# Performance work log

Hardware: AMD Instinct MI355X
Metric: run time of the kernel (lower is better)

## Reference

```python
import jax, jax.numpy as jnp
import numpy as np

B, N, C, H = 8, 1024, 768, 12
HD = C // H
SCALE = HD ** -0.5


def setup_inputs() -> dict:
    key = jax.random.key(0)
    k1, k2, k3 = jax.random.split(key, 3)
    x = jax.random.normal(k1, (B, N, C), dtype=jnp.float32)
    # parameter init roughly matching nn.Linear default scale
    w_qkv = jax.random.normal(k2, (C, 3 * C), dtype=jnp.float32) * (C ** -0.5)
    w_out = jax.random.normal(k3, (C, C), dtype=jnp.float32) * (C ** -0.5)
    b_out = jnp.zeros((C,), dtype=jnp.float32)
    return {"x": x, "w_qkv": w_qkv, "w_out": w_out, "b_out": b_out}


def reference(x, w_qkv, w_out, b_out):
    b, n, c = x.shape
    qkv = x @ w_qkv                                   # [b, n, 3c]
    q, k, v = jnp.split(qkv, 3, axis=-1)
    # [b, n, c] -> [b, heads, n, head_dim]
    def to_heads(t):
        return t.reshape(b, n, H, HD).transpose(0, 2, 1, 3)
    q, k, v = to_heads(q), to_heads(k), to_heads(v)
    dots = jnp.einsum('bhqd,bhkd->bhqk', q, k) * SCALE  # [b, h, n, n]
    attn = jax.nn.softmax(dots, axis=-1)
    # dropout is identity in eval mode
    out = jnp.einsum('bhqk,bhkd->bhqd', attn, v)        # [b, h, n, hd]
    out = out.transpose(0, 2, 1, 3).reshape(b, n, c)
    return out @ w_out + b_out
```

## Files before the change

### kernel.cpp

```cpp
#include <hip/hip_runtime.h>
#include <stdint.h>


typedef __attribute__((ext_vector_type(8))) __bf16 bf16x8;
typedef __attribute__((ext_vector_type(4))) float f32x4;

__device__ __forceinline__ uint16_t f2bf(float f) {
    union { float f; unsigned u; } c; c.f = f;
    unsigned x = c.u;
    unsigned r = (x + 0x7FFFu + ((x >> 16) & 1u)) >> 16;
    return (uint16_t)r;
}

__device__ __forceinline__ void gload_lds16(const uint16_t* g, uint16_t* l) {
    __builtin_amdgcn_global_load_lds(
        (const __attribute__((address_space(1))) unsigned int*)g,
        (__attribute__((address_space(3))) unsigned int*)l, 16, 0, 0);
}

__global__ __launch_bounds__(256) void cvt_f32_bf16(
    const float* __restrict__ src, uint16_t* __restrict__ dst, int n) {
    int i = (blockIdx.x * 256 + threadIdx.x) * 8;
    if (i + 8 > n) return;
    float4 a = *(const float4*)(src + i);
    float4 b = *(const float4*)(src + i + 4);
    union { uint16_t u[8]; uint4 v; } o;
    o.u[0] = f2bf(a.x); o.u[1] = f2bf(a.y); o.u[2] = f2bf(a.z); o.u[3] = f2bf(a.w);
    o.u[4] = f2bf(b.x); o.u[5] = f2bf(b.y); o.u[6] = f2bf(b.z); o.u[7] = f2bf(b.w);
    *(uint4*)(dst + i) = o.v;
}

__global__ void transpose_f32_bf16(const float* __restrict__ src,
                                   uint16_t* __restrict__ dst, int R, int Cc) {
    __shared__ uint16_t tile[32][33];
    int tx = threadIdx.x, ty = threadIdx.y;
    int c0 = blockIdx.x * 32, r0 = blockIdx.y * 32;
#pragma unroll
    for (int i = 0; i < 4; i++) {
        int r = ty + i * 8;
        tile[r][tx] = f2bf(src[(size_t)(r0 + r) * Cc + c0 + tx]);
    }
    __syncthreads();
#pragma unroll
    for (int i = 0; i < 4; i++) {
        int r = ty + i * 8;
        dst[(size_t)(c0 + r) * R + r0 + tx] = tile[tx][r];
    }
}

template <int MODE>
__global__ __launch_bounds__(256) void gemm128(
    const uint16_t* __restrict__ A, const uint16_t* __restrict__ Bt,
    int Kdim, int Ncols,
    uint16_t* __restrict__ qws, uint16_t* __restrict__ kws,
    uint16_t* __restrict__ vtws,
    const float* __restrict__ bias, float* __restrict__ outp) {
    __shared__ uint16_t lA[2][2][2048];
    __shared__ uint16_t lB[2][2][4096];

    int tid = threadIdx.x;
    int w = tid >> 6, lane = tid & 63, quad = lane >> 4, lo = lane & 15;
    int mw = w >> 1, nw = w & 1;
    int m0 = blockIdx.y * 64;
    int n0 = blockIdx.x * 128;

    int srow = tid >> 2;
    int skc = ((tid & 3) ^ ((tid >> 3) & 3)) * 8;
    const uint16_t* gA0 = A + (size_t)(m0 + srow) * Kdim + skc;
    const uint16_t* gB0 = Bt + (size_t)(n0 + srow) * Kdim + skc;
    const uint16_t* gB1 = gB0 + (size_t)64 * Kdim;

    f32x4 acc[2][4];
#pragma unroll
    for (int i = 0; i < 2; i++)
#pragma unroll
        for (int j = 0; j < 4; j++) acc[i][j] = (f32x4){0.f, 0.f, 0.f, 0.f};

    int swz = (quad ^ ((lo >> 1) & 3)) * 8;
    int aoff = (mw * 32 + lo) * 32 + swz;
    int boff = (nw * 64 + lo) * 32 + swz;

    const int nIter = Kdim >> 6;

#pragma unroll
    for (int s = 0; s < 2; s++) {
        gload_lds16(gA0 + s * 32, &lA[0][s][tid * 8]);
        gload_lds16(gB0 + s * 32, &lB[0][s][tid * 8]);
        gload_lds16(gB1 + s * 32, &lB[0][s][2048 + tid * 8]);
    }
    __syncthreads();

    for (int it = 0; it < nIter; it++) {
        const int cur = it & 1, nxt = cur ^ 1;
        const int kn = (it + 1 < nIter) ? (it + 1) * 64 : 0;

#pragma unroll
        for (int s = 0; s < 2; s++) {
            gload_lds16(gA0 + kn + s * 32, &lA[nxt][s][tid * 8]);
            gload_lds16(gB0 + kn + s * 32, &lB[nxt][s][tid * 8]);
            gload_lds16(gB1 + kn + s * 32, &lB[nxt][s][2048 + tid * 8]);
        }

#pragma unroll
        for (int s = 0; s < 2; s++) {
            bf16x8 af[2], bfr[4];
#pragma unroll
            for (int i = 0; i < 2; i++) af[i] = *(const bf16x8*)(&lA[cur][s][aoff + i * 512]);
#pragma unroll
            for (int j = 0; j < 4; j++) bfr[j] = *(const bf16x8*)(&lB[cur][s][boff + j * 512]);
#pragma unroll
            for (int i = 0; i < 2; i++)
#pragma unroll
                for (int j = 0; j < 4; j++)
                    acc[i][j] = __builtin_amdgcn_mfma_f32_16x16x32_bf16(
                        af[i], bfr[j], acc[i][j], 0, 0, 0);
        }
        __syncthreads();
    }

    if (MODE == 0) {
        int part = n0 / 768;
        int ccb = n0 % 768 + nw * 64;
        float qsc = (part == 0) ? 0.18033688011112042f : 1.0f;
#pragma unroll
        for (int i = 0; i < 2; i++)
#pragma unroll
            for (int j = 0; j < 4; j++)
#pragma unroll
                for (int r = 0; r < 4; r++) {
                    int m = m0 + mw * 32 + i * 16 + quad * 4 + r;
                    int bidx = m >> 10, nidx = m & 1023;
                    int cc = ccb + j * 16 + lo;
                    int h = cc >> 6, d = cc & 63;
                    int bh = bidx * 12 + h;
                    uint16_t v = f2bf(acc[i][j][r] * qsc);
                    int kt = nidx >> 5, keyin = nidx & 31;
                    if (part == 0) {
                        qws[((size_t)bh * 1024 + nidx) * 64 + d] = v;
                    } else if (part == 1) {
                        int fs = ((d >> 5) << 1) | (keyin & 1);
                        int idx = ((bh << 5) + kt) * 2048 + fs * 512 +
                                  ((((d & 31) >> 3) << 4) + (keyin >> 1)) * 8 + (d & 7);
                        kws[idx] = v;
                    } else {
                        int idx = ((bh << 5) + kt) * 2048 + (d >> 4) * 512 +
                                  (((keyin >> 3) << 4) + (d & 15)) * 8 + (keyin & 7);
                        vtws[idx] = v;
                    }
                }
    } else {
#pragma unroll
        for (int i = 0; i < 2; i++)
#pragma unroll
            for (int j = 0; j < 4; j++)
#pragma unroll
                for (int r = 0; r < 4; r++) {
                    int m = m0 + mw * 32 + i * 16 + quad * 4 + r;
                    int c = n0 + nw * 64 + j * 16 + lo;
                    outp[(size_t)m * Ncols + c] = acc[i][j][r] + bias[c];
                }
    }
}

__global__ __launch_bounds__(256) void attn_kernel(
    const uint16_t* __restrict__ qws, const uint16_t* __restrict__ kws,
    const uint16_t* __restrict__ vtws, uint16_t* __restrict__ attnout) {
    int bh = blockIdx.x;
    int qt = blockIdx.y;
    int tid = threadIdx.x;
    int w = tid >> 6, lane = tid & 63, quad = lane >> 4, lo = lane & 15;
    int q0 = qt * 128 + w * 32;

    const uint16_t* Qb = qws + (size_t)bh * 65536;
    const uint16_t* Kt = kws + (size_t)bh * 65536;
    const uint16_t* Vt = vtws + (size_t)bh * 65536;

    bf16x8 aq[2][2];
#pragma unroll
    for (int rg = 0; rg < 2; rg++)
#pragma unroll
        for (int h = 0; h < 2; h++)
            aq[rg][h] = *(const bf16x8*)(Qb + (size_t)(q0 + rg * 16 + lo) * 64 + h * 32 + quad * 8);

    f32x4 oacc[2][4], ol[2];
#pragma unroll
    for (int rg = 0; rg < 2; rg++) {
        ol[rg] = (f32x4){0.f, 0.f, 0.f, 0.f};
#pragma unroll
        for (int nd = 0; nd < 4; nd++) oacc[rg][nd] = (f32x4){0.f, 0.f, 0.f, 0.f};
    }

    bf16x8 ones;
#pragma unroll
    for (int i = 0; i < 8; i++) ones[i] = (__bf16)1.0f;

    __shared__ uint16_t P[4][2][16][40];

    const f32x4 zero4 = (f32x4){0.f, 0.f, 0.f, 0.f};

#pragma unroll 2
    for (int kt = 0; kt < 32; kt++) {
        const uint16_t* Kb = Kt + kt * 2048;
        const uint16_t* Vb = Vt + kt * 2048;

        bf16x8 bk[2][2], vv[4];
#pragma unroll
        for (int t = 0; t < 2; t++)
#pragma unroll
            for (int h = 0; h < 2; h++)
                bk[t][h] = *(const bf16x8*)(Kb + (h * 2 + t) * 512 + lane * 8);
#pragma unroll
        for (int nd = 0; nd < 4; nd++)
            vv[nd] = *(const bf16x8*)(Vb + nd * 512 + lane * 8);

#pragma unroll
        for (int rg = 0; rg < 2; rg++) {
            f32x4 s0 = __builtin_amdgcn_mfma_f32_16x16x32_bf16(aq[rg][0], bk[0][0], zero4, 0, 0, 0);
            s0 = __builtin_amdgcn_mfma_f32_16x16x32_bf16(aq[rg][1], bk[0][1], s0, 0, 0, 0);
            f32x4 s1 = __builtin_amdgcn_mfma_f32_16x16x32_bf16(aq[rg][0], bk[1][0], zero4, 0, 0, 0);
            s1 = __builtin_amdgcn_mfma_f32_16x16x32_bf16(aq[rg][1], bk[1][1], s1, 0, 0, 0);
#pragma unroll
            for (int r = 0; r < 4; r++) {
                union { float f; unsigned u; } u0, u1;
                u0.f = __builtin_exp2f(s0[r]);
                u1.f = __builtin_exp2f(s1[r]);
                unsigned pk = __builtin_amdgcn_perm(u1.u, u0.u, 0x07060302u);
                *(unsigned*)&P[w][rg][quad * 4 + r][2 * lo] = pk;
            }
        }

#pragma unroll
        for (int rg = 0; rg < 2; rg++) {
            bf16x8 ap = *(const bf16x8*)(&P[w][rg][lo][quad * 8]);
            ol[rg] = __builtin_amdgcn_mfma_f32_16x16x32_bf16(ap, ones, ol[rg], 0, 0, 0);
#pragma unroll
            for (int nd = 0; nd < 4; nd++)
                oacc[rg][nd] = __builtin_amdgcn_mfma_f32_16x16x32_bf16(ap, vv[nd], oacc[rg][nd], 0, 0, 0);
        }
    }

    int b = bh / 12, hh = bh % 12;
#pragma unroll
    for (int rg = 0; rg < 2; rg++)
#pragma unroll
        for (int r = 0; r < 4; r++) {
            float inv = 1.0f / ol[rg][r];
            int n = q0 + rg * 16 + quad * 4 + r;
            size_t base = ((size_t)(b * 1024 + n)) * 768 + hh * 64;
#pragma unroll
            for (int nd = 0; nd < 4; nd++)
                attnout[base + nd * 16 + lo] = f2bf(oacc[rg][nd][r] * inv);
        }
}

extern "C" void kernel_launch(void* const* d_in, const int* in_sizes, int n_in,
                              void* d_out, int out_size, void* d_ws, size_t ws_size,
                              hipStream_t stream) {
    const float* x     = (const float*)d_in[0];
    const float* w_qkv = (const float*)d_in[1];
    const float* w_out = (const float*)d_in[2];
    const float* b_out = (const float*)d_in[3];
    float* out = (float*)d_out;

    char* ws = (char*)d_ws;
    uint16_t* xbf   = (uint16_t*)(ws);
    uint16_t* qws   = (uint16_t*)(ws + 12582912);
    uint16_t* kws   = (uint16_t*)(ws + 25165824);
    uint16_t* vtws  = (uint16_t*)(ws + 37748736);
    uint16_t* attn  = (uint16_t*)(ws + 50331648);
    uint16_t* wtqkv = (uint16_t*)(ws + 62914560);
    uint16_t* wtout = (uint16_t*)(ws + 66453504);

    cvt_f32_bf16<<<6291456 / 2048, 256, 0, stream>>>(x, xbf, 6291456);

    transpose_f32_bf16<<<dim3(2304 / 32, 768 / 32), dim3(32, 8), 0, stream>>>(w_qkv, wtqkv, 768, 2304);
    transpose_f32_bf16<<<dim3(768 / 32, 768 / 32), dim3(32, 8), 0, stream>>>(w_out, wtout, 768, 768);

    gemm128<0><<<dim3(18, 128), 256, 0, stream>>>(
        xbf, wtqkv, 768, 2304, qws, kws, vtws, nullptr, nullptr);

    attn_kernel<<<dim3(96, 8), 256, 0, stream>>>(qws, kws, vtws, attn);

    gemm128<1><<<dim3(6, 128), 256, 0, stream>>>(
        attn, wtout, 768, 768, nullptr, nullptr, nullptr, b_out, out);
}
```

Measured before the change: 209.7 us.

## Merge prep kernels into one launch and swizzle GEMM workgroup order

Three preprocessing kernels (x conversion and two weight transposes) are folded into a single prep launch that dispatches by block index, removing two kernel launches and their gaps. The GEMM kernels also remap the linear workgroup id into an XCD-style interleaved order, so that blocks placed on the same chiplet work on neighbouring tiles and share L2. The remap assumes the grid size is divisible by 8, which holds for both GEMM launches.

New measurement: 198.8 us. 1.05x faster.

```diff
diff --git a/kernel.cpp b/kernel.cpp
--- a/kernel.cpp
+++ b/kernel.cpp
@@ -18,23 +18,38 @@
         (__attribute__((address_space(3))) unsigned int*)l, 16, 0, 0);
 }
 
-__global__ __launch_bounds__(256) void cvt_f32_bf16(
-    const float* __restrict__ src, uint16_t* __restrict__ dst, int n) {
-    int i = (blockIdx.x * 256 + threadIdx.x) * 8;
-    if (i + 8 > n) return;
-    float4 a = *(const float4*)(src + i);
-    float4 b = *(const float4*)(src + i + 4);
-    union { uint16_t u[8]; uint4 v; } o;
-    o.u[0] = f2bf(a.x); o.u[1] = f2bf(a.y); o.u[2] = f2bf(a.z); o.u[3] = f2bf(a.w);
-    o.u[4] = f2bf(b.x); o.u[5] = f2bf(b.y); o.u[6] = f2bf(b.z); o.u[7] = f2bf(b.w);
-    *(uint4*)(dst + i) = o.v;
-}
-
-__global__ void transpose_f32_bf16(const float* __restrict__ src,
-                                   uint16_t* __restrict__ dst, int R, int Cc) {
+__global__ __launch_bounds__(256) void prep(
+    const float* __restrict__ x, uint16_t* __restrict__ xbf,
+    const float* __restrict__ w_qkv, uint16_t* __restrict__ wtqkv,
+    const float* __restrict__ w_out, uint16_t* __restrict__ wtout) {
     __shared__ uint16_t tile[32][33];
-    int tx = threadIdx.x, ty = threadIdx.y;
-    int c0 = blockIdx.x * 32, r0 = blockIdx.y * 32;
+    int bid = blockIdx.x;
+    int tid = threadIdx.x;
+
+    if (bid < 3072) {
+        int i = (bid * 256 + tid) * 8;
+        float4 a = *(const float4*)(x + i);
+        float4 b = *(const float4*)(x + i + 4);
+        union { uint16_t u[8]; uint4 v; } o;
+        o.u[0] = f2bf(a.x); o.u[1] = f2bf(a.y); o.u[2] = f2bf(a.z); o.u[3] = f2bf(a.w);
+        o.u[4] = f2bf(b.x); o.u[5] = f2bf(b.y); o.u[6] = f2bf(b.z); o.u[7] = f2bf(b.w);
+        *(uint4*)(xbf + i) = o.v;
+        return;
+    }
+
+    const float* src; uint16_t* dst; int Cc, bx, by;
+    if (bid < 4800) {
+        int id = bid - 3072;
+        src = w_qkv; dst = wtqkv; Cc = 2304;
+        bx = id % 72; by = id / 72;
+    } else {
+        int id = bid - 4800;
+        src = w_out; dst = wtout; Cc = 768;
+        bx = id % 24; by = id / 24;
+    }
+    const int R = 768;
+    int tx = tid & 31, ty = tid >> 5;
+    int c0 = bx * 32, r0 = by * 32;
 #pragma unroll
     for (int i = 0; i < 4; i++) {
         int r = ty + i * 8;
@@ -61,8 +76,12 @@
     int tid = threadIdx.x;
     int w = tid >> 6, lane = tid & 63, quad = lane >> 4, lo = lane & 15;
     int mw = w >> 1, nw = w & 1;
-    int m0 = blockIdx.y * 64;
-    int n0 = blockIdx.x * 128;
+
+    int nwg = gridDim.x * gridDim.y;
+    int lid = blockIdx.y * gridDim.x + blockIdx.x;
+    int swzid = (lid & 7) * (nwg >> 3) + (lid >> 3);
+    int m0 = (swzid / gridDim.x) * 64;
+    int n0 = (swzid % gridDim.x) * 128;
 
     int srow = tid >> 2;
     int skc = ((tid & 3) ^ ((tid >> 3) & 3)) * 8;
@@ -271,10 +290,7 @@
     uint16_t* wtqkv = (uint16_t*)(ws + 62914560);
     uint16_t* wtout = (uint16_t*)(ws + 66453504);
 
-    cvt_f32_bf16<<<6291456 / 2048, 256, 0, stream>>>(x, xbf, 6291456);
-
-    transpose_f32_bf16<<<dim3(2304 / 32, 768 / 32), dim3(32, 8), 0, stream>>>(w_qkv, wtqkv, 768, 2304);
-    transpose_f32_bf16<<<dim3(768 / 32, 768 / 32), dim3(32, 8), 0, stream>>>(w_out, wtout, 768, 768);
+    prep<<<5376, 256, 0, stream>>>(x, xbf, w_qkv, wtqkv, w_out, wtout);
 
     gemm128<0><<<dim3(18, 128), 256, 0, stream>>>(
         xbf, wtqkv, 768, 2304, qws, kws, vtws, nullptr, nullptr);
```
